# Kernel tuning notes

Measured on AMD Instinct MI355X. Metric: run time of the kernel, lower is better.

The kernel has to match this reference:

```python
import jax, jax.numpy as jnp
import numpy as np

SIGMA_DIS = 3.0   # from init_kwargs
KMAX = 16         # max kernel label value (labels in 0..KMAX, 0 = background)


def setup_inputs() -> dict:
    key = jax.random.key(0)
    k1, k2 = jax.random.split(key)
    pred = jax.random.normal(k1, (16, 4, 640, 640), dtype=jnp.float32)
    labels = jax.random.randint(k2, (16, 640, 640), 0, KMAX + 1, dtype=jnp.int32)
    return {"pred_similarities": pred, "kernel_mask_ndi_labels": labels}


def _loss(pred, labels):
    # pred: (B, C, H, W) float; labels: (B, H, W) int in [0, KMAX]
    B, C = pred.shape[0], pred.shape[1]
    p = pred.reshape(B, C, -1)            # (B, C, P)
    lab = labels.reshape(B, -1)           # (B, P)
    sq = jnp.sum(p * p, axis=1)           # (B, P) per-pixel squared norm over channels

    # Per-segment sum of squared pred values and cardinality (scatter-reduce).
    seg_ss = jax.vmap(lambda s, l: jax.ops.segment_sum(s, l, num_segments=KMAX + 1))(sq, lab)            # (B, K+1)
    card = jax.vmap(lambda l: jax.ops.segment_sum(jnp.ones(l.shape, jnp.float32), l, num_segments=KMAX + 1))(lab)  # (B, K+1)

    # Masks for labels i and j are disjoint, so
    # ||pred*m_i/c_i - pred*m_j/c_j||_F^2 = SS_i/c_i^2 + SS_j/c_j^2 exactly.
    m = jnp.where(card > 0, seg_ss / jnp.square(jnp.maximum(card, 1.0)), 0.0)  # (B, K+1)

    ids = jnp.arange(KMAX + 1)
    pair_ok = (ids[:, None] >= 1) & (ids[None, :] > ids[:, None])               # i>=1, j>i
    valid = pair_ok[None, :, :] & (card[:, :, None] > 0) & (card[:, None, :] > 0)  # (B, K+1, K+1)

    s2 = m[:, :, None] + m[:, None, :]
    d = jnp.sqrt(jnp.where(valid, s2, 1.0))        # safe sqrt for masked-out pairs
    # NB: torch.max(norm, 0)[0] on a 0-dim tensor is the identity (no relu clamp) -> replicate.
    term = jnp.log1p(jnp.square(SIGMA_DIS - d))
    pair_sum = jnp.sum(jnp.where(valid, term, 0.0), axis=(1, 2))  # (B,)

    nk = jnp.max(lab, axis=1)                                      # num_kernels per image
    denom = (nk * (nk - 1)).astype(jnp.float32)
    loss_b = jnp.where(nk > 1, pair_sum / jnp.maximum(denom, 1.0), 0.0)
    return jnp.sum(loss_b)


def reference(pred_similarities, kernel_mask_ndi_labels):
    return _loss(pred_similarities, kernel_mask_ndi_labels)
```

## Files before the change

### kernel.cpp

```cpp
#include <hip/hip_runtime.h>

#define K   16
#define NB  16
#define NP  409600
#define NPV (NP / 4)
#define BX  64
#define NBLK (NB * BX)
#define SIGMA_DIS 3.0f

__global__ __launch_bounds__(256) void seg_reduce_kernel(
    const float* __restrict__ pred,
    const int*   __restrict__ lab,
    float* __restrict__ ss_part,
    float* __restrict__ cnt_part)
{
    __shared__ float2 bins[4][17][64];
    __shared__ float2 red[16][16];

    const int tid  = threadIdx.x;
    const int lane = tid & 63;
    const int wave = tid >> 6;
    const int b    = blockIdx.y;
    const int bx   = blockIdx.x;
    const int blk  = b * BX + bx;

    for (int e = tid; e < 4 * 17 * 64; e += 256)
        ((float2*)bins)[e] = make_float2(0.0f, 0.0f);
    __syncthreads();

    float2* mybin = &bins[wave][0][lane];

    const float4* p0 = (const float4*)(pred + ((size_t)b * 4 + 0) * NP);
    const float4* p1 = (const float4*)(pred + ((size_t)b * 4 + 1) * NP);
    const float4* p2 = (const float4*)(pred + ((size_t)b * 4 + 2) * NP);
    const float4* p3 = (const float4*)(pred + ((size_t)b * 4 + 3) * NP);
    const int4*   lb = (const int4*)(lab + (size_t)b * NP);

#pragma unroll 2
    for (int v = bx * 256 + tid; v < NPV; v += BX * 256) {
        float4 a = p0[v];
        float4 c = p1[v];
        float4 d = p2[v];
        float4 e = p3[v];
        int4   l = lb[v];

        float s0 = a.x * a.x + c.x * c.x + d.x * d.x + e.x * e.x;
        float s1 = a.y * a.y + c.y * c.y + d.y * d.y + e.y * e.y;
        float s2 = a.z * a.z + c.z * c.z + d.z * d.z + e.z * e.z;
        float s3 = a.w * a.w + c.w * c.w + d.w * d.w + e.w * e.w;

        { float2 t = mybin[l.x * 64]; t.x += s0; t.y += 1.0f; mybin[l.x * 64] = t; }
        { float2 t = mybin[l.y * 64]; t.x += s1; t.y += 1.0f; mybin[l.y * 64] = t; }
        { float2 t = mybin[l.z * 64]; t.x += s2; t.y += 1.0f; mybin[l.z * 64] = t; }
        { float2 t = mybin[l.w * 64]; t.x += s3; t.y += 1.0f; mybin[l.w * 64] = t; }
    }
    __syncthreads();

    {
        const int rk = (tid & 15) + 1;
        const int rs = tid >> 4;
        float2 acc = make_float2(0.0f, 0.0f);
#pragma unroll
        for (int j = 0; j < 16; ++j) {
            const int slot = rs + j * 16;
            float2 t = bins[slot >> 6][rk][slot & 63];
            acc.x += t.x;
            acc.y += t.y;
        }
        red[tid & 15][rs] = acc;
    }
    __syncthreads();

    if (tid < 16) {
        float ss = 0.0f, cc = 0.0f;
#pragma unroll
        for (int s = 0; s < 16; ++s) { ss += red[tid][s].x; cc += red[tid][s].y; }
        ss_part [tid * NBLK + blk] = ss;
        cnt_part[tid * NBLK + blk] = cc;
    }
}

__global__ __launch_bounds__(256) void finalize_kernel(
    const float* __restrict__ ss_part,
    const float* __restrict__ cnt_part,
    float* __restrict__ out)
{
    __shared__ float m_sh[NB][K];
    __shared__ float c_sh[NB][K];
    __shared__ float inv_denom[NB];
    __shared__ float red[256];

    const int t = threadIdx.x;

    {
        const int fb = t >> 4;
        const int fk = t & 15;
        const float4* sp = (const float4*)(ss_part  + fk * NBLK + fb * BX);
        const float4* cp = (const float4*)(cnt_part + fk * NBLK + fb * BX);
        float ss = 0.0f, cc = 0.0f;
#pragma unroll
        for (int i = 0; i < BX / 4; ++i) {
            float4 v = sp[i];
            float4 w = cp[i];
            ss += v.x + v.y + v.z + v.w;
            cc += w.x + w.y + w.z + w.w;
        }
        c_sh[fb][fk] = cc;
        m_sh[fb][fk] = (cc > 0.0f) ? ss / (cc * cc) : 0.0f;
    }
    __syncthreads();

    if (t < NB) {
        int nk = 0;
        for (int k = K; k >= 1; --k) {
            if (c_sh[t][k - 1] > 0.0f) { nk = k; break; }
        }
        float denom = (float)(nk * (nk - 1));
        inv_denom[t] = (nk > 1) ? 1.0f / fmaxf(denom, 1.0f) : 0.0f;
    }
    __syncthreads();

    float acc = 0.0f;
    for (int e = t; e < NB * K * K; e += 256) {
        const int fb = e >> 8;
        const int ij = e & 255;
        const int ki = ij >> 4;
        const int kj = ij & 15;
        if (kj > ki && c_sh[fb][ki] > 0.0f && c_sh[fb][kj] > 0.0f) {
            float s2 = m_sh[fb][ki] + m_sh[fb][kj];
            float dd = sqrtf(s2);
            float x  = SIGMA_DIS - dd;
            acc += log1pf(x * x) * inv_denom[fb];
        }
    }

    red[t] = acc;
    __syncthreads();
    for (int s = 128; s > 0; s >>= 1) {
        if (t < s) red[t] += red[t + s];
        __syncthreads();
    }
    if (t == 0) out[0] = red[0];
}

extern "C" void kernel_launch(void* const* d_in, const int* in_sizes, int n_in,
                              void* d_out, int out_size, void* d_ws, size_t ws_size,
                              hipStream_t stream) {
    const float* pred = (const float*)d_in[0];
    const int*   lab  = (const int*)d_in[1];
    float* out = (float*)d_out;

    float* ss_part  = (float*)d_ws;
    float* cnt_part = ss_part + K * NBLK;

    dim3 grid(BX, NB);
    seg_reduce_kernel<<<grid, 256, 0, stream>>>(pred, lab, ss_part, cnt_part);
    finalize_kernel<<<1, 256, 0, stream>>>(ss_part, cnt_part, out);
}
```

Before: 41.44 us.

## Share LDS bins across wave pairs with atomics and double the grid

Per-wave private float2 histogram bins become two sets of split float bins (sum and count), each shared by two waves and updated with LDS atomicAdd. The grid's x-dimension doubles to 128 blocks per image and the unroll pragma is dropped. This shrinks LDS per block and adds more blocks in flight to hide global memory latency, at the cost of atomic LDS traffic and contention from 256 updates landing on the same lane column. Finalize reads more partials.

```diff
diff --git a/kernel.cpp b/kernel.cpp
--- a/kernel.cpp
+++ b/kernel.cpp
@@ -4,7 +4,7 @@
 #define NB  16
 #define NP  409600
 #define NPV (NP / 4)
-#define BX  64
+#define BX  128
 #define NBLK (NB * BX)
 #define SIGMA_DIS 3.0f
 
@@ -14,21 +14,25 @@
     float* __restrict__ ss_part,
     float* __restrict__ cnt_part)
 {
-    __shared__ float2 bins[4][17][64];
+    __shared__ float ss_h [2][17 * 64];
+    __shared__ float cnt_h[2][17 * 64];
     __shared__ float2 red[16][16];
 
     const int tid  = threadIdx.x;
     const int lane = tid & 63;
-    const int wave = tid >> 6;
+    const int set  = tid >> 7;
     const int b    = blockIdx.y;
     const int bx   = blockIdx.x;
     const int blk  = b * BX + bx;
 
-    for (int e = tid; e < 4 * 17 * 64; e += 256)
-        ((float2*)bins)[e] = make_float2(0.0f, 0.0f);
+    for (int e = tid; e < 2 * 17 * 64; e += 256) {
+        (&ss_h [0][0])[e] = 0.0f;
+        (&cnt_h[0][0])[e] = 0.0f;
+    }
     __syncthreads();
 
-    float2* mybin = &bins[wave][0][lane];
+    float* ssl  = &ss_h [set][lane];
+    float* cntl = &cnt_h[set][lane];
 
     const float4* p0 = (const float4*)(pred + ((size_t)b * 4 + 0) * NP);
     const float4* p1 = (const float4*)(pred + ((size_t)b * 4 + 1) * NP);
@@ -36,7 +40,6 @@
     const float4* p3 = (const float4*)(pred + ((size_t)b * 4 + 3) * NP);
     const int4*   lb = (const int4*)(lab + (size_t)b * NP);
 
-#pragma unroll 2
     for (int v = bx * 256 + tid; v < NPV; v += BX * 256) {
         float4 a = p0[v];
         float4 c = p1[v];
@@ -49,25 +52,24 @@
         float s2 = a.z * a.z + c.z * c.z + d.z * d.z + e.z * e.z;
         float s3 = a.w * a.w + c.w * c.w + d.w * d.w + e.w * e.w;
 
-        { float2 t = mybin[l.x * 64]; t.x += s0; t.y += 1.0f; mybin[l.x * 64] = t; }
-        { float2 t = mybin[l.y * 64]; t.x += s1; t.y += 1.0f; mybin[l.y * 64] = t; }
-        { float2 t = mybin[l.z * 64]; t.x += s2; t.y += 1.0f; mybin[l.z * 64] = t; }
-        { float2 t = mybin[l.w * 64]; t.x += s3; t.y += 1.0f; mybin[l.w * 64] = t; }
+        atomicAdd(&ssl [l.x * 64], s0);  atomicAdd(&cntl[l.x * 64], 1.0f);
+        atomicAdd(&ssl [l.y * 64], s1);  atomicAdd(&cntl[l.y * 64], 1.0f);
+        atomicAdd(&ssl [l.z * 64], s2);  atomicAdd(&cntl[l.z * 64], 1.0f);
+        atomicAdd(&ssl [l.w * 64], s3);  atomicAdd(&cntl[l.w * 64], 1.0f);
     }
     __syncthreads();
 
     {
         const int rk = (tid & 15) + 1;
         const int rs = tid >> 4;
-        float2 acc = make_float2(0.0f, 0.0f);
+        float ssa = 0.0f, cca = 0.0f;
 #pragma unroll
-        for (int j = 0; j < 16; ++j) {
-            const int slot = rs + j * 16;
-            float2 t = bins[slot >> 6][rk][slot & 63];
-            acc.x += t.x;
-            acc.y += t.y;
+        for (int j = 0; j < 8; ++j) {
+            const int slot = rs * 8 + j;
+            ssa += ss_h [slot >> 6][rk * 64 + (slot & 63)];
+            cca += cnt_h[slot >> 6][rk * 64 + (slot & 63)];
         }
-        red[tid & 15][rs] = acc;
+        red[tid & 15][rs] = make_float2(ssa, cca);
     }
     __syncthreads();
 
```

Result: slower. 110.1 us (+165.7%).
